# Performance work log

Measured on AMD Instinct MI355X. Metric: run time of the kernel, lower is better.

The kernel has to match this reference:

```python
import jax, jax.numpy as jnp
import numpy as np

EMBED_DIM = 2048
N_HEADS = 32
N_GROUPS = 8
HEAD_SIZE = EMBED_DIM // N_HEADS  # 64
SCALE = HEAD_SIZE ** -0.5
B, S = 2, 2048


def setup_inputs() -> dict:
    key = jax.random.key(0)
    ks = jax.random.split(key, 7)
    kv_dim = N_GROUPS * HEAD_SIZE
    x = jax.random.normal(ks[0], (B, S, EMBED_DIM), dtype=jnp.float32)
    # Linear weights stored [in, out] (y = x @ W), matching torch nn.Linear math.
    Wq = jax.random.normal(ks[1], (EMBED_DIM, EMBED_DIM), dtype=jnp.float32) * (EMBED_DIM ** -0.5)
    Wk = jax.random.normal(ks[2], (EMBED_DIM, kv_dim), dtype=jnp.float32) * (EMBED_DIM ** -0.5)
    Wv = jax.random.normal(ks[3], (EMBED_DIM, kv_dim), dtype=jnp.float32) * (EMBED_DIM ** -0.5)
    Wo = jax.random.normal(ks[4], (EMBED_DIM, EMBED_DIM), dtype=jnp.float32) * (EMBED_DIM ** -0.5)
    bo = jnp.zeros((EMBED_DIM,), dtype=jnp.float32)
    # causal boolean mask [S, S], broadcast over batch and heads
    mask = jnp.tril(jnp.ones((S, S), dtype=jnp.bool_))
    return {"x": x, "Wq": Wq, "Wk": Wk, "Wv": Wv, "Wo": Wo, "bo": bo, "mask": mask}


def reference(x, Wq, Wk, Wv, Wo, bo, mask):
    B_, S_, E = x.shape
    q = (x @ Wq).reshape(B_, S_, N_HEADS, HEAD_SIZE).transpose(0, 2, 1, 3)   # [B,H,S,D]
    k = (x @ Wk).reshape(B_, S_, N_GROUPS, HEAD_SIZE).transpose(0, 2, 1, 3)  # [B,G,S,D]
    v = (x @ Wv).reshape(B_, S_, N_GROUPS, HEAD_SIZE).transpose(0, 2, 1, 3)
    # GQA: each KV head serves H//G consecutive query heads (matches torch expand+reshape)
    rep = N_HEADS // N_GROUPS
    k = jnp.repeat(k, rep, axis=1)  # [B,H,S,D]
    v = jnp.repeat(v, rep, axis=1)
    scores = SCALE * jnp.einsum("bhqd,bhkd->bhqk", q, k)          # [B,H,S,S]
    scores = jnp.where(mask, scores, -jnp.inf)
    weights = jax.nn.softmax(scores, axis=-1)                      # dropout in eval mode (identity)
    attn = jnp.einsum("bhqk,bhkd->bhqd", weights, v)               # [B,H,S,D]
    attn = attn.transpose(0, 2, 1, 3).reshape(B_, S_, E)
    return attn @ Wo + bo
```

## Files before the change

kernel.cpp:

```cpp
#include <hip/hip_runtime.h>
#include <hip/hip_fp16.h>

#define E_DIM 2048
#define S_LEN 2048
#define NH 32
#define HD 64
#define KV_DIM 512
#define QKV_N 3072
#define M_ROWS 4096
#define QK_SCALE 0.18033688011112042f

typedef __bf16 bf16x8 __attribute__((ext_vector_type(8)));
typedef float f32x4 __attribute__((ext_vector_type(4)));

__device__ __forceinline__ void async_lds16(const __bf16* g, __bf16* l) {
    __builtin_amdgcn_global_load_lds(
        (const __attribute__((address_space(1))) void*)g,
        (__attribute__((address_space(3))) void*)l, 16, 0, 0);
}

__global__ void k_convert(const float* __restrict__ x, __bf16* __restrict__ xb, int n) {
    int i = (blockIdx.x * blockDim.x + threadIdx.x) * 4;
    if (i < n) {
        float4 v = *(const float4*)(x + i);
        xb[i + 0] = (__bf16)v.x;
        xb[i + 1] = (__bf16)v.y;
        xb[i + 2] = (__bf16)v.z;
        xb[i + 3] = (__bf16)v.w;
    }
}

__global__ void k_transpose_all(const float* __restrict__ Wq, const float* __restrict__ Wk,
                                const float* __restrict__ Wv, const float* __restrict__ Wo,
                                __bf16* __restrict__ WtAll, __bf16* __restrict__ WoT) {
    const int which = blockIdx.z;
    const float* W;
    __bf16* dst;
    int N;
    float scale = 1.f;
    if (which == 0)      { W = Wq; dst = WtAll;                                    N = E_DIM;  scale = QK_SCALE; }
    else if (which == 1) { W = Wk; dst = WtAll + (size_t)E_DIM * E_DIM;            N = KV_DIM; }
    else if (which == 2) { W = Wv; dst = WtAll + (size_t)(E_DIM + KV_DIM) * E_DIM; N = KV_DIM; }
    else                 { W = Wo; dst = WoT;                                      N = E_DIM;  }
    const int n0 = blockIdx.x * 32;
    if (n0 >= N) return;
    const int k0 = blockIdx.y * 32;
    __shared__ float tile[32][33];
    int tx = threadIdx.x, ty = threadIdx.y;
#pragma unroll
    for (int j = 0; j < 4; ++j)
        tile[ty + j * 8][tx] = W[(size_t)(k0 + ty + j * 8) * N + n0 + tx];
    __syncthreads();
#pragma unroll
    for (int j = 0; j < 4; ++j)
        dst[(size_t)(n0 + ty + j * 8) * E_DIM + k0 + tx] = (__bf16)(tile[tx][ty + j * 8] * scale);
}

template <int OUT_F32>
__global__ __launch_bounds__(256, 2)
void k_gemm_bt(const __bf16* __restrict__ A, const __bf16* __restrict__ Bt,
               void* __restrict__ Cout, const float* __restrict__ bias,
               int M, int N, int K) {
    __shared__ __attribute__((aligned(16))) __bf16 As[128 * 64];
    __shared__ __attribute__((aligned(16))) __bf16 Bs[128 * 64];
    const int t = threadIdx.x;
    const int lane = t & 63, wave = t >> 6;
    const int quad = lane >> 4, l16 = lane & 15;
    const int wr = wave >> 1, wc = wave & 1;
    const int m0 = blockIdx.y * 128, n0 = blockIdx.x * 128;

    const int srow = t >> 2;
    const int sblk = (t & 3) ^ ((t >> 3) & 3);
    const __bf16* gA0 = A + (size_t)(m0 + srow) * K + sblk * 8;
    const __bf16* gA1 = gA0 + (size_t)64 * K;
    const __bf16* gB0 = Bt + (size_t)(n0 + srow) * K + sblk * 8;
    const __bf16* gB1 = gB0 + (size_t)64 * K;

    f32x4 acc[4][4] = {};

    for (int k0 = 0; k0 < K; k0 += 64) {
#pragma unroll
        for (int ks = 0; ks < 2; ++ks) {
            async_lds16(gA0 + k0 + ks * 32, As + ks * 4096 + wave * 512);
            async_lds16(gA1 + k0 + ks * 32, As + ks * 4096 + 2048 + wave * 512);
            async_lds16(gB0 + k0 + ks * 32, Bs + ks * 4096 + wave * 512);
            async_lds16(gB1 + k0 + ks * 32, Bs + ks * 4096 + 2048 + wave * 512);
        }
        __syncthreads();
#pragma unroll
        for (int ks = 0; ks < 2; ++ks) {
            bf16x8 af[4], bfr[4];
#pragma unroll
            for (int i = 0; i < 4; ++i) {
                const int row = wr * 64 + i * 16 + l16;
                af[i] = *(const bf16x8*)((const char*)As + ks * 8192 + row * 64 +
                                         ((quad ^ ((row >> 1) & 3)) * 16));
            }
#pragma unroll
            for (int j = 0; j < 4; ++j) {
                const int row = wc * 64 + j * 16 + l16;
                bfr[j] = *(const bf16x8*)((const char*)Bs + ks * 8192 + row * 64 +
                                          ((quad ^ ((row >> 1) & 3)) * 16));
            }
#pragma unroll
            for (int i = 0; i < 4; ++i)
#pragma unroll
                for (int j = 0; j < 4; ++j)
                    acc[i][j] = __builtin_amdgcn_mfma_f32_16x16x32_bf16(af[i], bfr[j], acc[i][j], 0, 0, 0);
        }
        __syncthreads();
    }

#pragma unroll
    for (int i = 0; i < 4; ++i)
#pragma unroll
        for (int j = 0; j < 4; ++j) {
            const int row = m0 + wr * 64 + i * 16 + quad * 4;
            const int col = n0 + wc * 64 + j * 16 + l16;
#pragma unroll
            for (int r = 0; r < 4; ++r) {
                float v = acc[i][j][r];
                if (OUT_F32) ((float*)Cout)[(size_t)(row + r) * N + col] = v + bias[col];
                else ((__bf16*)Cout)[(size_t)(row + r) * N + col] = (__bf16)v;
            }
        }
}

__global__ __launch_bounds__(256, 3)
void k_attn(const __bf16* __restrict__ qkv, __half* __restrict__ partO,
            float* __restrict__ partL) {
    const int xr = (int)(gridDim.x - 1 - blockIdx.x);
    int qi, c;
    if (xr < 8)       { qi = xr;                  c = 0; }
    else if (xr < 24) { qi = 8 + ((xr - 8) >> 1); c = (xr - 8) & 1; }
    else if (xr < 48) { qi = 16 + (xr - 24) / 3;  c = (xr - 24) % 3; }
    else              { qi = 24 + ((xr - 48) >> 2); c = (xr - 48) & 3; }
    const int q0 = qi * 64;
    const int k_lo = c * 512;
    const int k_hi = min(k_lo + 512, q0 + 64);

    const int gp = blockIdx.y;
    const int g = gp >> 1;
    const int h0 = g * 4 + (gp & 1) * 2;
    const int b = blockIdx.z;
    const int t = threadIdx.x;
    const int lane = t & 63, wave = t >> 6;
    const int quad = lane >> 4, l16 = lane & 15;

    __shared__ __attribute__((aligned(16))) __bf16 Kls[128 * 64];
    __shared__ __attribute__((aligned(16))) __bf16 vT[64][136];
    __shared__ __attribute__((aligned(16))) __bf16 pT[4][2][1024];

    const __bf16* base = qkv + (size_t)b * S_LEN * QKV_N;
    const int qrow = q0 + wave * 16 + l16;

    bf16x8 qf[2][2];
#pragma unroll
    for (int h = 0; h < 2; ++h)
#pragma unroll
        for (int s = 0; s < 2; ++s)
            qf[h][s] = *(const bf16x8*)(base + (size_t)qrow * QKV_N + (h0 + h) * HD + s * 32 + quad * 8);

    f32x4 o[2][4] = {};
    float l_st[2] = {0.f, 0.f};

    const int vkey = lane * 2, vdg = wave * 16;
    const __bf16* vsrc = base + (E_DIM + KV_DIM) + g * HD + vdg;
    const __bf16* ksrc = base + E_DIM + g * HD;

    const int klocal = lane >> 3;
    const int kdblk = (lane & 7) ^ (klocal & 7);
    const __bf16* gk_base = ksrc + (size_t)(wave * 32 + klocal) * QKV_N + kdblk * 8;
    __bf16* lk_base = Kls + wave * 2048;

    auto qk = [&](int m, f32x4* sA, f32x4* sB) {
#pragma unroll
        for (int kt = 0; kt < 4; ++kt) {
            const int kr = m * 64 + kt * 16 + l16;
            const char* kb_ = (const char*)Kls + kr * 128;
            bf16x8 kf0 = *(const bf16x8*)(kb_ + ((quad ^ (kr & 7)) * 16));
            bf16x8 kf1 = *(const bf16x8*)(kb_ + (((4 + quad) ^ (kr & 7)) * 16));
            f32x4 z = {};
            z = __builtin_amdgcn_mfma_f32_16x16x32_bf16(kf0, qf[0][0], z, 0, 0, 0);
            sA[kt] = __builtin_amdgcn_mfma_f32_16x16x32_bf16(kf1, qf[0][1], z, 0, 0, 0);
            f32x4 w = {};
            w = __builtin_amdgcn_mfma_f32_16x16x32_bf16(kf0, qf[1][0], w, 0, 0, 0);
            sB[kt] = __builtin_amdgcn_mfma_f32_16x16x32_bf16(kf1, qf[1][1], w, 0, 0, 0);
        }
    };

    auto softmax_p = [&](int kb, int h, f32x4* sc) {
        const bool diag = (kb == q0);
        char* prow = (char*)&pT[wave][h][0] + l16 * 128;
        float lsum = 0.f;
#pragma unroll
        for (int kt = 0; kt < 4; ++kt) {
            f32x4 p;
#pragma unroll
            for (int r = 0; r < 4; ++r) p[r] = exp2f(sc[kt][r]);
            if (diag) {
                const int kbase = kb + kt * 16 + quad * 4;
#pragma unroll
                for (int r = 0; r < 4; ++r)
                    if (kbase + r > qrow) p[r] = 0.f;
            }
#pragma unroll
            for (int r = 0; r < 4; ++r) lsum += p[r];
            __bf16 pb[4];
#pragma unroll
            for (int r = 0; r < 4; ++r) pb[r] = (__bf16)p[r];
            *(uint2*)(prow + ((2 * kt + (quad >> 1)) ^ (l16 & 7)) * 16 + (quad & 1) * 8) =
                *(const uint2*)pb;
        }
        l_st[h] += lsum;
    };

    auto pv = [&](int m) {
        bf16x8 vf[4][2];
        const int koff = m * 64;
#pragma unroll
        for (int cc = 0; cc < 4; ++cc)
#pragma unroll
            for (int kh = 0; kh < 2; ++kh)
                vf[cc][kh] = *(const bf16x8*)&vT[cc * 16 + l16][koff + kh * 32 + quad * 8];
#pragma unroll
        for (int h = 0; h < 2; ++h) {
            const char* prow = (const char*)&pT[wave][h][0] + l16 * 128;
            bf16x8 pf0 = *(const bf16x8*)(prow + ((0 + quad) ^ (l16 & 7)) * 16);
            bf16x8 pf1 = *(const bf16x8*)(prow + ((4 + quad) ^ (l16 & 7)) * 16);
#pragma unroll
            for (int cc = 0; cc < 4; ++cc) {
                o[h][cc] = __builtin_amdgcn_mfma_f32_16x16x32_bf16(vf[cc][0], pf0, o[h][cc], 0, 0, 0);
                o[h][cc] = __builtin_amdgcn_mfma_f32_16x16x32_bf16(vf[cc][1], pf1, o[h][cc], 0, 0, 0);
            }
        }
    };

    for (int kv0 = k_lo; kv0 < k_hi; kv0 += 128) {
#pragma unroll
        for (int i = 0; i < 4; ++i)
            async_lds16(gk_base + (size_t)(kv0 + i * 8) * QKV_N, lk_base + i * 512);

        const __bf16* vp = vsrc + (size_t)(kv0 + vkey) * QKV_N;
        uint4 va0 = *(const uint4*)(vp);
        uint4 va1 = *(const uint4*)(vp + 8);
        uint4 vb0 = *(const uint4*)(vp + QKV_N);
        uint4 vb1 = *(const uint4*)(vp + QKV_N + 8);

        {
            const unsigned short* a0 = (const unsigned short*)&va0;
            const unsigned short* a1 = (const unsigned short*)&va1;
            const unsigned short* b0 = (const unsigned short*)&vb0;
            const unsigned short* b1 = (const unsigned short*)&vb1;
#pragma unroll
            for (int j = 0; j < 8; ++j) {
                *(uint32_t*)&vT[vdg + j][vkey] = (uint32_t)a0[j] | ((uint32_t)b0[j] << 16);
                *(uint32_t*)&vT[vdg + 8 + j][vkey] = (uint32_t)a1[j] | ((uint32_t)b1[j] << 16);
            }
        }
        __syncthreads();

        f32x4 scA[4], scB[4];
        qk(0, scA, scB);
        softmax_p(kv0, 0, scA);
        softmax_p(kv0, 1, scB);
        pv(0);

        const int kb1 = kv0 + 64;
        if (kb1 < k_hi) {
            qk(1, scA, scB);
            softmax_p(kb1, 0, scA);
            softmax_p(kb1, 1, scB);
            pv(1);
        }
        __syncthreads();
    }

    const size_t blk = ((size_t)b * 16 + gp) * 80 + xr;
    const size_t pb = blk * (2 * 64 * 64);
#pragma unroll
    for (int h = 0; h < 2; ++h) {
        float lt = l_st[h];
        lt += __shfl_xor(lt, 16);
        lt += __shfl_xor(lt, 32);
        const float inv = 1.f / lt;
        __half* prow = partO + pb + (size_t)(h * 64 + wave * 16 + l16) * 64 + quad * 4;
#pragma unroll
        for (int dt = 0; dt < 4; ++dt) {
            __half ob[4];
#pragma unroll
            for (int r = 0; r < 4; ++r) ob[r] = __float2half(o[h][dt][r] * inv);
            *(uint2*)(prow + dt * 16) = *(const uint2*)ob;
        }
        if (quad == 0)
            partL[blk * 128 + h * 64 + wave * 16 + l16] = lt;
    }
}

__global__ __launch_bounds__(256, 4)
void k_combine(const __half* __restrict__ partO, const float* __restrict__ partL,
               __bf16* __restrict__ attnb) {
    const int qi = blockIdx.x, gp = blockIdx.y, b = blockIdx.z;
    const int nc = (qi >> 3) + 1;
    int x0;
    if (qi < 8) x0 = qi;
    else if (qi < 16) x0 = 8 + (qi - 8) * 2;
    else if (qi < 24) x0 = 24 + (qi - 16) * 3;
    else x0 = 48 + (qi - 24) * 4;

    const int t = threadIdx.x;
    const int row = t >> 1, half = t & 1;
    const int h = row >> 6, q = row & 63;
    const int d0 = half * 32;
    const size_t gbase = ((size_t)b * 16 + gp) * 80;

    float W = 0.f;
    float acc[32];
#pragma unroll
    for (int i = 0; i < 32; ++i) acc[i] = 0.f;
    for (int cc = 0; cc < nc; ++cc) {
        const float a = partL[(gbase + x0 + cc) * 128 + h * 64 + q];
        W += a;
        const __half* src = partO + (gbase + x0 + cc) * (2 * 64 * 64) + (size_t)(h * 64 + q) * 64 + d0;
#pragma unroll
        for (int i = 0; i < 32; i += 8) {
            uint4 u = *(const uint4*)(src + i);
            const __half* hs = (const __half*)&u;
#pragma unroll
            for (int j = 0; j < 8; ++j) acc[i + j] += a * __half2float(hs[j]);
        }
    }
    const float inv = 1.f / W;
    const int h_abs = (gp >> 1) * 4 + (gp & 1) * 2 + h;
    __bf16* dst = attnb + ((size_t)b * S_LEN + qi * 64 + q) * E_DIM + h_abs * 64 + d0;
#pragma unroll
    for (int i = 0; i < 32; i += 8) {
        __bf16 ob[8];
#pragma unroll
        for (int j = 0; j < 8; ++j) ob[j] = (__bf16)(acc[i + j] * inv);
        *(uint4*)(dst + i) = *(const uint4*)ob;
    }
}

extern "C" void kernel_launch(void* const* d_in, const int* in_sizes, int n_in,
                              void* d_out, int out_size, void* d_ws, size_t ws_size,
                              hipStream_t stream) {
    const float* x  = (const float*)d_in[0];
    const float* Wq = (const float*)d_in[1];
    const float* Wk = (const float*)d_in[2];
    const float* Wv = (const float*)d_in[3];
    const float* Wo = (const float*)d_in[4];
    const float* bo = (const float*)d_in[5];

    __bf16* xb    = (__bf16*)d_ws;
    __bf16* WtAll = xb + (size_t)M_ROWS * E_DIM;
    __bf16* WoT   = WtAll + (size_t)QKV_N * E_DIM;
    __bf16* qkv   = WoT + (size_t)E_DIM * E_DIM;
    __bf16* attnb = qkv + (size_t)M_ROWS * QKV_N;
    __half* partO = (__half*)(attnb + (size_t)M_ROWS * E_DIM);
    float* partL  = (float*)(partO + (size_t)2560 * 2 * 64 * 64);

    k_convert<<<(M_ROWS * E_DIM / 4 + 255) / 256, 256, 0, stream>>>(x, xb, M_ROWS * E_DIM);
    k_transpose_all<<<dim3(64, 64, 4), dim3(32, 8), 0, stream>>>(Wq, Wk, Wv, Wo, WtAll, WoT);

    k_gemm_bt<0><<<dim3(QKV_N / 128, M_ROWS / 128), 256, 0, stream>>>(
        xb, WtAll, (void*)qkv, nullptr, M_ROWS, QKV_N, E_DIM);

    k_attn<<<dim3(80, 16, 2), 256, 0, stream>>>(qkv, partO, partL);
    k_combine<<<dim3(32, 16, 2), 256, 0, stream>>>(partO, partL, attnb);

    k_gemm_bt<1><<<dim3(E_DIM / 128, M_ROWS / 128), 256, 0, stream>>>(
        attnb, WoT, d_out, bo, M_ROWS, E_DIM, E_DIM);
}
```

Measured before the change: 341.9 us.

## Halve LDS tiles in GEMM and attention to raise occupancy

The GEMM K-step drops from 64 to 32, halving its LDS footprint, and launch bounds go from 2 to 3 blocks per CU. The attention kernel now handles 64 keys per iteration instead of 128, with smaller K, V-transpose and P buffers (P shared across the two heads), and its launch bounds go from 3 to 4. The aim is more resident waves to hide memory latency. In exchange both kernels hit barriers twice as often per unit of work, do less compute per synchronisation, and may be forced into tighter register budgets that can cause spills.

```diff
diff --git a/kernel.cpp b/kernel.cpp
--- a/kernel.cpp
+++ b/kernel.cpp
@@ -57,12 +57,12 @@
 }
 
 template <int OUT_F32>
-__global__ __launch_bounds__(256, 2)
+__global__ __launch_bounds__(256, 3)
 void k_gemm_bt(const __bf16* __restrict__ A, const __bf16* __restrict__ Bt,
                void* __restrict__ Cout, const float* __restrict__ bias,
                int M, int N, int K) {
-    __shared__ __attribute__((aligned(16))) __bf16 As[128 * 64];
-    __shared__ __attribute__((aligned(16))) __bf16 Bs[128 * 64];
+    __shared__ __attribute__((aligned(16))) __bf16 As[128 * 32];
+    __shared__ __attribute__((aligned(16))) __bf16 Bs[128 * 32];
     const int t = threadIdx.x;
     const int lane = t & 63, wave = t >> 6;
     const int quad = lane >> 4, l16 = lane & 15;
@@ -75,39 +75,35 @@
     const __bf16* gA1 = gA0 + (size_t)64 * K;
     const __bf16* gB0 = Bt + (size_t)(n0 + srow) * K + sblk * 8;
     const __bf16* gB1 = gB0 + (size_t)64 * K;
+    __bf16* lA0 = As + wave * 512;
+    __bf16* lA1 = As + 2048 + wave * 512;
+    __bf16* lB0 = Bs + wave * 512;
+    __bf16* lB1 = Bs + 2048 + wave * 512;
 
     f32x4 acc[4][4] = {};
 
-    for (int k0 = 0; k0 < K; k0 += 64) {
-#pragma unroll
-        for (int ks = 0; ks < 2; ++ks) {
-            async_lds16(gA0 + k0 + ks * 32, As + ks * 4096 + wave * 512);
-            async_lds16(gA1 + k0 + ks * 32, As + ks * 4096 + 2048 + wave * 512);
-            async_lds16(gB0 + k0 + ks * 32, Bs + ks * 4096 + wave * 512);
-            async_lds16(gB1 + k0 + ks * 32, Bs + ks * 4096 + 2048 + wave * 512);
-        }
+    for (int k0 = 0; k0 < K; k0 += 32) {
+        async_lds16(gA0 + k0, lA0);
+        async_lds16(gA1 + k0, lA1);
+        async_lds16(gB0 + k0, lB0);
+        async_lds16(gB1 + k0, lB1);
         __syncthreads();
-#pragma unroll
-        for (int ks = 0; ks < 2; ++ks) {
-            bf16x8 af[4], bfr[4];
-#pragma unroll
-            for (int i = 0; i < 4; ++i) {
-                const int row = wr * 64 + i * 16 + l16;
-                af[i] = *(const bf16x8*)((const char*)As + ks * 8192 + row * 64 +
-                                         ((quad ^ ((row >> 1) & 3)) * 16));
-            }
-#pragma unroll
-            for (int j = 0; j < 4; ++j) {
-                const int row = wc * 64 + j * 16 + l16;
-                bfr[j] = *(const bf16x8*)((const char*)Bs + ks * 8192 + row * 64 +
-                                          ((quad ^ ((row >> 1) & 3)) * 16));
-            }
-#pragma unroll
-            for (int i = 0; i < 4; ++i)
-#pragma unroll
-                for (int j = 0; j < 4; ++j)
-                    acc[i][j] = __builtin_amdgcn_mfma_f32_16x16x32_bf16(af[i], bfr[j], acc[i][j], 0, 0, 0);
-        }
+        bf16x8 af[4], bfr[4];
+#pragma unroll
+        for (int i = 0; i < 4; ++i) {
+            const int row = wr * 64 + i * 16 + l16;
+            af[i] = *(const bf16x8*)((const char*)As + row * 64 + ((quad ^ ((row >> 1) & 3)) * 16));
+        }
+#pragma unroll
+        for (int j = 0; j < 4; ++j) {
+            const int row = wc * 64 + j * 16 + l16;
+            bfr[j] = *(const bf16x8*)((const char*)Bs + row * 64 + ((quad ^ ((row >> 1) & 3)) * 16));
+        }
+#pragma unroll
+        for (int i = 0; i < 4; ++i)
+#pragma unroll
+            for (int j = 0; j < 4; ++j)
+                acc[i][j] = __builtin_amdgcn_mfma_f32_16x16x32_bf16(af[i], bfr[j], acc[i][j], 0, 0, 0);
         __syncthreads();
     }
 
@@ -126,7 +122,7 @@
         }
 }
 
-__global__ __launch_bounds__(256, 3)
+__global__ __launch_bounds__(256, 4)
 void k_attn(const __bf16* __restrict__ qkv, __half* __restrict__ partO,
             float* __restrict__ partL) {
     const int xr = (int)(gridDim.x - 1 - blockIdx.x);
@@ -147,9 +143,9 @@
     const int lane = t & 63, wave = t >> 6;
     const int quad = lane >> 4, l16 = lane & 15;
 
-    __shared__ __attribute__((aligned(16))) __bf16 Kls[128 * 64];
-    __shared__ __attribute__((aligned(16))) __bf16 vT[64][136];
-    __shared__ __attribute__((aligned(16))) __bf16 pT[4][2][1024];
+    __shared__ __attribute__((aligned(16))) __bf16 Kls[64 * 64];
+    __shared__ __attribute__((aligned(16))) __bf16 vT[64][68];
+    __shared__ __attribute__((aligned(16))) __bf16 pT[4][1024];
 
     const __bf16* base = qkv + (size_t)b * S_LEN * QKV_N;
     const int qrow = q0 + wave * 16 + l16;
@@ -164,19 +160,20 @@
     f32x4 o[2][4] = {};
     float l_st[2] = {0.f, 0.f};
 
-    const int vkey = lane * 2, vdg = wave * 16;
-    const __bf16* vsrc = base + (E_DIM + KV_DIM) + g * HD + vdg;
     const __bf16* ksrc = base + E_DIM + g * HD;
-
     const int klocal = lane >> 3;
     const int kdblk = (lane & 7) ^ (klocal & 7);
-    const __bf16* gk_base = ksrc + (size_t)(wave * 32 + klocal) * QKV_N + kdblk * 8;
-    __bf16* lk_base = Kls + wave * 2048;
-
-    auto qk = [&](int m, f32x4* sA, f32x4* sB) {
+    const __bf16* gk0 = ksrc + (size_t)(wave * 16 + klocal) * QKV_N + kdblk * 8;
+    __bf16* lk0 = Kls + wave * 16 * 64;
+
+    const int vkey = (lane & 31) * 2;
+    const int vd0 = wave * 16 + (lane >> 5) * 8;
+    const __bf16* vsrc = base + (E_DIM + KV_DIM) + g * HD + vd0;
+
+    auto qk = [&](f32x4* sA, f32x4* sB) {
 #pragma unroll
         for (int kt = 0; kt < 4; ++kt) {
-            const int kr = m * 64 + kt * 16 + l16;
+            const int kr = kt * 16 + l16;
             const char* kb_ = (const char*)Kls + kr * 128;
             bf16x8 kf0 = *(const bf16x8*)(kb_ + ((quad ^ (kr & 7)) * 16));
             bf16x8 kf1 = *(const bf16x8*)(kb_ + (((4 + quad) ^ (kr & 7)) * 16));
@@ -191,7 +188,7 @@
 
     auto softmax_p = [&](int kb, int h, f32x4* sc) {
         const bool diag = (kb == q0);
-        char* prow = (char*)&pT[wave][h][0] + l16 * 128;
+        char* prow = (char*)&pT[wave][0] + l16 * 128;
         float lsum = 0.f;
 #pragma unroll
         for (int kt = 0; kt < 4; ++kt) {
@@ -215,64 +212,47 @@
         l_st[h] += lsum;
     };
 
-    auto pv = [&](int m) {
+    auto pv = [&](int h, const bf16x8 vf[4][2]) {
+        const char* prow = (const char*)&pT[wave][0] + l16 * 128;
+        bf16x8 pf0 = *(const bf16x8*)(prow + ((0 + quad) ^ (l16 & 7)) * 16);
+        bf16x8 pf1 = *(const bf16x8*)(prow + ((4 + quad) ^ (l16 & 7)) * 16);
+#pragma unroll
+        for (int cc = 0; cc < 4; ++cc) {
+            o[h][cc] = __builtin_amdgcn_mfma_f32_16x16x32_bf16(vf[cc][0], pf0, o[h][cc], 0, 0, 0);
+            o[h][cc] = __builtin_amdgcn_mfma_f32_16x16x32_bf16(vf[cc][1], pf1, o[h][cc], 0, 0, 0);
+        }
+    };
+
+    for (int kv0 = k_lo; kv0 < k_hi; kv0 += 64) {
+        async_lds16(gk0 + (size_t)kv0 * QKV_N, lk0);
+        async_lds16(gk0 + (size_t)(kv0 + 8) * QKV_N, lk0 + 8 * 64);
+
+        const __bf16* vp = vsrc + (size_t)(kv0 + vkey) * QKV_N;
+        uint4 va = *(const uint4*)(vp);
+        uint4 vb = *(const uint4*)(vp + QKV_N);
+        {
+            const unsigned short* a = (const unsigned short*)&va;
+            const unsigned short* bb = (const unsigned short*)&vb;
+#pragma unroll
+            for (int j = 0; j < 8; ++j)
+                *(uint32_t*)&vT[vd0 + j][vkey] = (uint32_t)a[j] | ((uint32_t)bb[j] << 16);
+        }
+        __syncthreads();
+
+        f32x4 scA[4], scB[4];
+        qk(scA, scB);
+
         bf16x8 vf[4][2];
-        const int koff = m * 64;
 #pragma unroll
         for (int cc = 0; cc < 4; ++cc)
 #pragma unroll
             for (int kh = 0; kh < 2; ++kh)
-                vf[cc][kh] = *(const bf16x8*)&vT[cc * 16 + l16][koff + kh * 32 + quad * 8];
-#pragma unroll
-        for (int h = 0; h < 2; ++h) {
-            const char* prow = (const char*)&pT[wave][h][0] + l16 * 128;
-            bf16x8 pf0 = *(const bf16x8*)(prow + ((0 + quad) ^ (l16 & 7)) * 16);
-            bf16x8 pf1 = *(const bf16x8*)(prow + ((4 + quad) ^ (l16 & 7)) * 16);
-#pragma unroll
-            for (int cc = 0; cc < 4; ++cc) {
-                o[h][cc] = __builtin_amdgcn_mfma_f32_16x16x32_bf16(vf[cc][0], pf0, o[h][cc], 0, 0, 0);
-                o[h][cc] = __builtin_amdgcn_mfma_f32_16x16x32_bf16(vf[cc][1], pf1, o[h][cc], 0, 0, 0);
-            }
-        }
-    };
-
-    for (int kv0 = k_lo; kv0 < k_hi; kv0 += 128) {
-#pragma unroll
-        for (int i = 0; i < 4; ++i)
-            async_lds16(gk_base + (size_t)(kv0 + i * 8) * QKV_N, lk_base + i * 512);
-
-        const __bf16* vp = vsrc + (size_t)(kv0 + vkey) * QKV_N;
-        uint4 va0 = *(const uint4*)(vp);
-        uint4 va1 = *(const uint4*)(vp + 8);
-        uint4 vb0 = *(const uint4*)(vp + QKV_N);
-        uint4 vb1 = *(const uint4*)(vp + QKV_N + 8);
-
-        {
-            const unsigned short* a0 = (const unsigned short*)&va0;
-            const unsigned short* a1 = (const unsigned short*)&va1;
-            const unsigned short* b0 = (const unsigned short*)&vb0;
-            const unsigned short* b1 = (const unsigned short*)&vb1;
-#pragma unroll
-            for (int j = 0; j < 8; ++j) {
-                *(uint32_t*)&vT[vdg + j][vkey] = (uint32_t)a0[j] | ((uint32_t)b0[j] << 16);
-                *(uint32_t*)&vT[vdg + 8 + j][vkey] = (uint32_t)a1[j] | ((uint32_t)b1[j] << 16);
-            }
-        }
-        __syncthreads();
-
-        f32x4 scA[4], scB[4];
-        qk(0, scA, scB);
+                vf[cc][kh] = *(const bf16x8*)&vT[cc * 16 + l16][kh * 32 + quad * 8];
+
         softmax_p(kv0, 0, scA);
+        pv(0, vf);
         softmax_p(kv0, 1, scB);
-        pv(0);
-
-        const int kb1 = kv0 + 64;
-        if (kb1 < k_hi) {
-            qk(1, scA, scB);
-            softmax_p(kb1, 0, scA);
-            softmax_p(kb1, 1, scB);
-            pv(1);
-        }
+        pv(1, vf);
         __syncthreads();
     }
 
```

Measured after the change: 351.4 us. +2.8%, slower.
